# Kernel tuning notes

Measured on AMD Instinct MI355X. Metric: run time of the kernel, lower is better.

The kernel has to match this reference:

```python
import jax, jax.numpy as jnp
import numpy as np
import math

IMG_SIZE = 768
NUM_CLASSES = 90
THRESHOLD = 0.05
IOU_THRESHOLD = 0.5
MAX_DETECTIONS = 100
K_CAND = 512  # per-class candidate pool before greedy NMS
RATIOS = [(1.0, 1.0), (1.4, 0.7), (0.7, 1.4)]
SCALES = [2 ** 0, 2 ** (1.0 / 3.0), 2 ** (2.0 / 3.0)]


def _generate_anchors():
    anchor_scale = 4.0
    pyramid_levels = [3, 4, 5, 6, 7]
    all_levels = []
    for lv in pyramid_levels:
        stride = 2 ** lv
        size = anchor_scale * 2 ** lv
        grid = IMG_SIZE // stride
        sx = np.arange(grid) * stride
        sy, sx = np.meshgrid(np.arange(grid) * stride, sx, indexing='ij')
        # torch meshgrid(shift_y, shift_x, indexing='ij') -> rows are y
        yy, xx = np.meshgrid(np.arange(grid) * stride, np.arange(grid) * stride, indexing='ij')
        shifts = np.stack([xx.ravel(), yy.ravel(), xx.ravel(), yy.ravel()], axis=1).astype(np.float32)
        base = []
        for r in RATIOS:
            for s in SCALES:
                w = size * s * math.sqrt(r[0] / r[1])
                h = size * s * math.sqrt(r[1] / r[0])
                base.append([-w / 2, -h / 2, w / 2, h / 2])
        base = np.asarray(base, dtype=np.float32)  # [9,4]
        anc = (base[None, :, :] + shifts[:, None, :]).reshape(-1, 4)
        all_levels.append(anc)
    return np.concatenate(all_levels, axis=0)  # [110484,4]


def setup_inputs() -> dict:
    key = jax.random.key(0)
    k1, k2, k3 = jax.random.split(key, 3)
    A = 110484
    x = jax.random.normal(k1, (1, 3, IMG_SIZE, IMG_SIZE), dtype=jnp.float32)
    regression = jax.random.normal(k2, (1, A, 4), dtype=jnp.float32) * 0.3
    classification = jax.random.normal(k3, (1, A, NUM_CLASSES), dtype=jnp.float32) - 2.0
    anchors = jnp.asarray(_generate_anchors())
    return {"x": x, "regression": regression, "classification": classification, "anchors": anchors}


def _decode_and_clip(anchors, deltas, H, W):
    # BBoxTransform (RetinaNet-style): deltas = (dx, dy, dw, dh)
    wa = anchors[:, 2] - anchors[:, 0]
    ha = anchors[:, 3] - anchors[:, 1]
    cxa = anchors[:, 0] + 0.5 * wa
    cya = anchors[:, 1] + 0.5 * ha
    dx, dy, dw, dh = deltas[:, 0], deltas[:, 1], deltas[:, 2], deltas[:, 3]
    cx = cxa + dx * wa
    cy = cya + dy * ha
    w = jnp.exp(dw) * wa
    h = jnp.exp(dh) * ha
    x1 = jnp.clip(cx - 0.5 * w, 0.0, W)
    y1 = jnp.clip(cy - 0.5 * h, 0.0, H)
    x2 = jnp.clip(cx + 0.5 * w, 0.0, W)
    y2 = jnp.clip(cy + 0.5 * h, 0.0, H)
    return jnp.stack([x1, y1, x2, y2], axis=1)  # [A,4]


def _pairwise_iou(b):  # [K,4] -> [K,K]
    area = (b[:, 2] - b[:, 0]) * (b[:, 3] - b[:, 1])
    xx1 = jnp.maximum(b[:, None, 0], b[None, :, 0])
    yy1 = jnp.maximum(b[:, None, 1], b[None, :, 1])
    xx2 = jnp.minimum(b[:, None, 2], b[None, :, 2])
    yy2 = jnp.minimum(b[:, None, 3], b[None, :, 3])
    inter = jnp.clip(xx2 - xx1, 0.0) * jnp.clip(yy2 - yy1, 0.0)
    return inter / (area[:, None] + area[None, :] - inter + 1e-8)


def _greedy_nms(iou_c, valid_c):
    # boxes are pre-sorted by descending score; fixed-iteration greedy NMS
    def step(suppressed, i):
        keep_i = valid_c[i] & jnp.logical_not(suppressed[i])
        suppressed = jnp.where(keep_i, suppressed | (iou_c[i] > IOU_THRESHOLD), suppressed)
        return suppressed, keep_i
    _, keep = jax.lax.scan(step, jnp.zeros(iou_c.shape[0], dtype=bool), jnp.arange(iou_c.shape[0]))
    return keep  # [K]


def _postprocess(x, regression, classification, anchors):
    H, W = x.shape[2], x.shape[3]
    boxes = _decode_and_clip(anchors, regression[0], float(H), float(W))  # [A,4]
    scores = jax.nn.sigmoid(classification[0])                            # [A,C]
    # per-class top-K candidate pool (sorted desc), fixed-shape NMS
    vals, idx = jax.lax.top_k(scores.T, K_CAND)        # [C,K]
    cand = boxes[idx]                                   # [C,K,4]
    valid = vals > THRESHOLD                            # [C,K]
    iou = jax.vmap(_pairwise_iou)(cand)                 # [C,K,K]
    keep = jax.vmap(_greedy_nms)(iou, valid)            # [C,K]
    kept_scores = jnp.where(keep, vals, -1.0).reshape(-1)  # [C*K]
    top_vals, flat_idx = jax.lax.top_k(kept_scores, MAX_DETECTIONS)
    labels = (flat_idx // K_CAND).astype(jnp.float32)
    det_boxes = cand.reshape(-1, 4)[flat_idx]
    ok = top_vals > 0.0
    det = jnp.concatenate([
        jnp.zeros((MAX_DETECTIONS, 1), dtype=jnp.float32),  # batch ids (batch=1 -> 0)
        det_boxes,
        top_vals[:, None],
        labels[:, None],
    ], axis=1)  # [100,7]
    return jnp.where(ok[:, None], det, 0.0)


def reference(x, regression, classification, anchors):
    return _postprocess(x, regression, classification, anchors)
```

## Files before the change

kernel.cpp:

```cpp
#include <hip/hip_runtime.h>
#include <math.h>


#define A_N   110484
#define C_N   90
#define KCAND 512
#define NBINS 8192
#define KSH   19
#define MAXDET 100
#define IMG_F 768.0f
#define THRESH 0.05f
#define NS    4
#define VTOT  (A_N / 4)
#define VS4   ((VTOT + NS - 1) / NS)
#define SL_CAP 1024
#define CAND_N (NS * KCAND)
#define KEEP_CAP 100
#define T_BLKS ((A_N + 63) / 64)
#define S_BLKS (C_N * NS)
#define D_BLKS ((A_N + 255) / 256)
#define FCAP  512

typedef unsigned int u32;
typedef unsigned long long u64;

__device__ __forceinline__ u32 fkey(float f) {
    u32 u = __float_as_uint(f);
    return (u & 0x80000000u) ? ~u : (u | 0x80000000u);
}
__device__ __forceinline__ float unfkey(u32 k) {
    u32 u = (k & 0x80000000u) ? (k ^ 0x80000000u) : ~k;
    return __uint_as_float(u);
}
__device__ __forceinline__ u64 shflx64(u64 v, int m) {
    u32 lo = (u32)__shfl_xor((int)(u32)v, m, 64);
    u32 hi = (u32)__shfl_xor((int)(v >> 32), m, 64);
    return ((u64)hi << 32) | lo;
}

__global__ __launch_bounds__(256)
void prep_kernel(const float* __restrict__ cls,
                 u32* __restrict__ keysT) {
    __shared__ u32 tile[64 * 91];
    const int a0 = blockIdx.x * 64;
    const int lim = min(64, A_N - a0);
    const int n4 = (lim * C_N) >> 2;
    const float4* src4 = (const float4*)(cls + (size_t)a0 * C_N);
    for (int i4 = threadIdx.x; i4 < n4; i4 += 256) {
        float4 x4 = src4[i4];
        const u32 base = (u32)(4 * i4);
        float xs[4] = { x4.x, x4.y, x4.z, x4.w };
        #pragma unroll
        for (int k = 0; k < 4; ++k) {
            u32 i = base + k;
            u32 aa = i / C_N, c = i % C_N;
            float s = 1.0f / (1.0f + expf(-xs[k]));
            tile[aa * 91 + c] = fkey(s);
        }
    }
    __syncthreads();
    for (int j = threadIdx.x; j < C_N * 64; j += 256) {
        int c = j >> 6, aa = j & 63;
        if (aa < lim)
            keysT[(size_t)c * A_N + a0 + aa] = tile[aa * 91 + c];
    }
}

__global__ __launch_bounds__(256)
void select_kernel(const u32* __restrict__ keysT,
                   const float* __restrict__ anchors,
                   const float* __restrict__ reg,
                   float4* __restrict__ boxes,
                   u64* __restrict__ candbuf) {
    __shared__ u32 hist[NBINS];
    __shared__ u32 csum[256];
    __shared__ u64 lbuf[SL_CAP];
    __shared__ u32 sPv;
    __shared__ int lcnt;
    const int tid = threadIdx.x;

    if (blockIdx.x >= S_BLKS) {
        int a = (blockIdx.x - S_BLKS) * 256 + tid;
        if (a < A_N) {
            float4 an = ((const float4*)anchors)[a];
            float4 dl = ((const float4*)reg)[a];
            float wa = an.z - an.x, ha = an.w - an.y;
            float cx = an.x + 0.5f * wa + dl.x * wa;
            float cy = an.y + 0.5f * ha + dl.y * ha;
            float w = expf(dl.z) * wa;
            float h = expf(dl.w) * ha;
            float4 o;
            o.x = fminf(fmaxf(cx - 0.5f * w, 0.0f), IMG_F);
            o.y = fminf(fmaxf(cy - 0.5f * h, 0.0f), IMG_F);
            o.z = fminf(fmaxf(cx + 0.5f * w, 0.0f), IMG_F);
            o.w = fminf(fmaxf(cy + 0.5f * h, 0.0f), IMG_F);
            boxes[a] = o;
        }
        return;
    }
    const int c = blockIdx.x >> 2, s = blockIdx.x & 3;
    const int lo = s * VS4, hiEnd = min(VTOT, lo + VS4);
    const uint4* kv = (const uint4*)(keysT + (size_t)c * A_N);

    for (int i = tid; i < NBINS; i += 256) hist[i] = 0;
    if (tid == 0) { sPv = 0; lcnt = 0; }
    __syncthreads();
    for (int i = lo + tid; i < hiEnd; i += 256) {
        uint4 k = kv[i];
        atomicAdd(&hist[k.x >> KSH], 1u);
        atomicAdd(&hist[k.y >> KSH], 1u);
        atomicAdd(&hist[k.z >> KSH], 1u);
        atomicAdd(&hist[k.w >> KSH], 1u);
    }
    __syncthreads();
    u32 own = 0; const int hi = NBINS - 1 - 32 * tid;
    #pragma unroll 4
    for (int j = 0; j < 32; ++j) own += hist[hi - j];
    csum[tid] = own;
    __syncthreads();
    for (int off = 1; off < 256; off <<= 1) {
        u32 v = csum[tid];
        u32 a = (tid >= off) ? csum[tid - off] : 0u;
        __syncthreads();
        csum[tid] = v + a;
        __syncthreads();
    }
    const u32 incl = csum[tid], excl = incl - own;
    if (excl < (u32)KCAND && incl >= (u32)KCAND) {
        u32 cum = excl;
        for (int j = 0; j < 32; ++j) {
            u32 hv = hist[hi - j];
            if (cum + hv >= (u32)KCAND) { sPv = (u32)(hi - j); break; }
            cum += hv;
        }
    }
    __syncthreads();
    const u32 P = sPv;
    for (int i = lo + tid; i < hiEnd; i += 256) {
        uint4 k = kv[i];
        u32 base = (u32)(4 * i);
        if ((k.x >> KSH) >= P) {
            int p = atomicAdd(&lcnt, 1);
            if (p < SL_CAP) lbuf[p] = (((u64)(~k.x)) << 32) | base;
        }
        if ((k.y >> KSH) >= P) {
            int p = atomicAdd(&lcnt, 1);
            if (p < SL_CAP) lbuf[p] = (((u64)(~k.y)) << 32) | (base + 1);
        }
        if ((k.z >> KSH) >= P) {
            int p = atomicAdd(&lcnt, 1);
            if (p < SL_CAP) lbuf[p] = (((u64)(~k.z)) << 32) | (base + 2);
        }
        if ((k.w >> KSH) >= P) {
            int p = atomicAdd(&lcnt, 1);
            if (p < SL_CAP) lbuf[p] = (((u64)(~k.w)) << 32) | (base + 3);
        }
    }
    __syncthreads();
    const int n = min(lcnt, SL_CAP);
    for (int i = tid; i < SL_CAP; i += 256) if (i >= n) lbuf[i] = ~0ULL;
    __syncthreads();

    {
        const int l = tid & 63, w = tid >> 6;
        int ii[4]; u64 v[4];
        #pragma unroll
        for (int r = 0; r < 4; ++r) { ii[r] = 256 * w + 64 * r + l; v[r] = lbuf[ii[r]]; }
        __syncthreads();
        #pragma unroll
        for (u32 kk = 2; kk <= 1024; kk <<= 1) {
            #pragma unroll
            for (u32 j = kk >> 1; j > 0; j >>= 1) {
                if (j >= 256) {
                    #pragma unroll
                    for (int r = 0; r < 4; ++r) lbuf[ii[r]] = v[r];
                    __syncthreads();
                    #pragma unroll
                    for (int r = 0; r < 4; ++r) {
                        u64 pv = lbuf[ii[r] ^ j];
                        bool up = ((ii[r] & kk) == 0);
                        bool m = (((ii[r] & j) == 0) == up);
                        v[r] = m ? (v[r] < pv ? v[r] : pv) : (v[r] > pv ? v[r] : pv);
                    }
                    __syncthreads();
                } else if (j >= 64) {
                    const int rx = (int)(j >> 6);
                    u64 nv[4];
                    #pragma unroll
                    for (int r = 0; r < 4; ++r) {
                        u64 pv = v[r ^ rx];
                        bool up = ((ii[r] & kk) == 0);
                        bool m = (((ii[r] & j) == 0) == up);
                        nv[r] = m ? (v[r] < pv ? v[r] : pv) : (v[r] > pv ? v[r] : pv);
                    }
                    #pragma unroll
                    for (int r = 0; r < 4; ++r) v[r] = nv[r];
                } else {
                    #pragma unroll
                    for (int r = 0; r < 4; ++r) {
                        u64 pv = shflx64(v[r], (int)j);
                        bool up = ((ii[r] & kk) == 0);
                        bool m = (((ii[r] & j) == 0) == up);
                        v[r] = m ? (v[r] < pv ? v[r] : pv) : (v[r] > pv ? v[r] : pv);
                    }
                }
            }
        }
        u64* cb = candbuf + (size_t)c * CAND_N + (size_t)s * KCAND;
        const bool rev = (s & 1);
        #pragma unroll
        for (int r = 0; r < 4; ++r) {
            if (ii[r] < KCAND) {
                int d = rev ? (KCAND - 1 - ii[r]) : ii[r];
                cb[d] = v[r];
            }
        }
    }
}

__global__ __launch_bounds__(1024)
void snms_kernel(const u64* __restrict__ candbuf,
                 const float4* __restrict__ boxes,
                 u32* __restrict__ keptbuf, u32* __restrict__ cnt2) {
    __shared__ u64 sortbuf[2][CAND_N];
    __shared__ float bxx[KCAND], byy[KCAND], bzz[KCAND], bww[KCAND];
    __shared__ float ar[KCAND], sc[KCAND];
    __shared__ u32 keepf[16], wbase[17];
    u32* bmask = (u32*)&sortbuf[0][0];
    const int c = blockIdx.x, tid = threadIdx.x;
    const int l = tid & 63, w = tid >> 6;
    const int i0 = 128 * w + l, i1 = i0 + 64;

    const u64* cb = candbuf + (size_t)c * CAND_N;
    u64 v0 = cb[i0], v1 = cb[i1];
    int p = 0;
    #pragma unroll
    for (u32 kk = 1024; kk <= (u32)CAND_N; kk <<= 1) {
        #pragma unroll
        for (u32 j = kk >> 1; j > 0; j >>= 1) {
            if (j >= 128) {
                sortbuf[p][i0] = v0; sortbuf[p][i1] = v1;
                __syncthreads();
                u64 w0 = sortbuf[p][i0 ^ j], w1 = sortbuf[p][i1 ^ j];
                bool m0 = (((i0 & j) == 0) == ((i0 & kk) == 0));
                bool m1 = (((i1 & j) == 0) == ((i1 & kk) == 0));
                v0 = m0 ? (v0 < w0 ? v0 : w0) : (v0 > w0 ? v0 : w0);
                v1 = m1 ? (v1 < w1 ? v1 : w1) : (v1 > w1 ? v1 : w1);
                p ^= 1;
            } else if (j == 64) {
                bool up = ((i0 & kk) == 0);
                u64 mn = v0 < v1 ? v0 : v1, mx = v0 < v1 ? v1 : v0;
                v0 = up ? mn : mx; v1 = up ? mx : mn;
            } else {
                u64 w0 = shflx64(v0, (int)j), w1 = shflx64(v1, (int)j);
                bool m0 = (((i0 & j) == 0) == ((i0 & kk) == 0));
                bool m1 = (((i1 & j) == 0) == ((i1 & kk) == 0));
                v0 = m0 ? (v0 < w0 ? v0 : w0) : (v0 > w0 ? v0 : w0);
                v1 = m1 ? (v1 < w1 ? v1 : w1) : (v1 > w1 ? v1 : w1);
            }
        }
    }
    __syncthreads();

    if (w < 4) {
        u32 idx0 = (u32)v0, key0 = ~((u32)(v0 >> 32));
        u32 idx1 = (u32)v1, key1 = ~((u32)(v1 >> 32));
        sc[i0] = unfkey(key0); sc[i1] = unfkey(key1);
        float4 b0 = boxes[idx0], b1 = boxes[idx1];
        bxx[i0] = b0.x; byy[i0] = b0.y; bzz[i0] = b0.z; bww[i0] = b0.w;
        bxx[i1] = b1.x; byy[i1] = b1.y; bzz[i1] = b1.z; bww[i1] = b1.w;
        ar[i0] = (b0.z - b0.x) * (b0.w - b0.y);
        ar[i1] = (b1.z - b1.x) * (b1.w - b1.y);
    }
    for (int i = tid; i < KCAND * 16; i += 1024) bmask[i] = 0;
    if (tid < 16) keepf[tid] = 0;
    __syncthreads();

    {
        const int i = tid & (KCAND - 1);
        const int half = tid >> 9;
        const int count = (KCAND - 1) - i;
        const int j0 = i + 1 + (half ? (count >> 1) : 0);
        const int j1 = half ? KCAND : (i + 1 + (count >> 1));
        const float bix = bxx[i], biy = byy[i], biz = bzz[i], biw = bww[i];
        const float ai = ar[i];
        u32 m[16];
        #pragma unroll
        for (int q = 0; q < 16; ++q) m[q] = 0;
        for (int j = j0; j < j1; ++j) {
            float xx1 = fmaxf(bix, bxx[j]), yy1 = fmaxf(biy, byy[j]);
            float xx2 = fminf(biz, bzz[j]), yy2 = fminf(biw, bww[j]);
            float inter = fmaxf(xx2 - xx1, 0.0f) * fmaxf(yy2 - yy1, 0.0f);
            float uni = ai + ar[j] - inter + 1e-8f;
            if (inter > 0.5f * uni) m[j >> 5] |= (1u << (j & 31));
        }
        #pragma unroll
        for (int q = 0; q < 16; ++q)
            if (m[q]) atomicOr(&bmask[i * 16 + q], m[q]);
    }
    __syncthreads();

    if (tid < 64) {
        const int lw = tid & 15;
        u32 removed = 0, keepw = 0;
        u32 rA[8], rB[8]; float sA[8], sB[8];
        #pragma unroll
        for (int k = 0; k < 8; ++k) { rA[k] = bmask[k * 16 + lw]; sA[k] = sc[k]; }
        #pragma unroll 1
        for (int ch = 0; ch < 64; ch += 2) {
            const int tb1 = (ch + 1) * 8;
            #pragma unroll
            for (int k = 0; k < 8; ++k) { rB[k] = bmask[(tb1 + k) * 16 + lw]; sB[k] = sc[tb1 + k]; }
            {
                const int tb = ch * 8;
                #pragma unroll
                for (int k = 0; k < 8; ++k) {
                    const int t = tb + k;
                    u32 rw = (u32)__builtin_amdgcn_readlane((int)removed, t >> 5);
                    bool d = (sA[k] > THRESH) && (((rw >> (t & 31)) & 1u) == 0u);
                    removed |= d ? rA[k] : 0u;
                    keepw |= (d && (tid == (t >> 5))) ? (1u << (t & 31)) : 0u;
                }
            }
            const int tb2 = (ch + 2 < 64) ? (ch + 2) * 8 : 0;
            #pragma unroll
            for (int k = 0; k < 8; ++k) { rA[k] = bmask[(tb2 + k) * 16 + lw]; sA[k] = sc[tb2 + k]; }
            {
                #pragma unroll
                for (int k = 0; k < 8; ++k) {
                    const int t = tb1 + k;
                    u32 rw = (u32)__builtin_amdgcn_readlane((int)removed, t >> 5);
                    bool d = (sB[k] > THRESH) && (((rw >> (t & 31)) & 1u) == 0u);
                    removed |= d ? rB[k] : 0u;
                    keepw |= (d && (tid == (t >> 5))) ? (1u << (t & 31)) : 0u;
                }
            }
        }
        if (tid < 16) keepf[tid] = keepw;
    }
    __syncthreads();

    if (tid == 0) {
        u32 t = 0;
        for (int q = 0; q < 16; ++q) { wbase[q] = t; t += __popc(keepf[q]); }
        wbase[16] = t;
        cnt2[c] = (t < (u32)KEEP_CAP) ? t : (u32)KEEP_CAP;
    }
    __syncthreads();
    if (tid < KCAND) {
        u32 word = keepf[tid >> 5];
        u32 bit = (u32)tid & 31u;
        if ((word >> bit) & 1u) {
            u32 rank = wbase[tid >> 5] + __popc(word & ((1u << bit) - 1u));
            if (rank < (u32)KEEP_CAP) {
                float s = sc[tid];
                uint4 a, b;
                a.x = ~fkey(s);
                a.y = (u32)(c * KCAND + tid);
                a.z = __float_as_uint(bxx[tid]);
                a.w = __float_as_uint(byy[tid]);
                b.x = __float_as_uint(bzz[tid]);
                b.y = __float_as_uint(bww[tid]);
                b.z = __float_as_uint(s);
                b.w = 0u;
                uint4* e = (uint4*)(keptbuf + ((size_t)c * KEEP_CAP + rank) * 8);
                e[0] = a; e[1] = b;
            }
        }
    }
}

__global__ __launch_bounds__(1024)
void final_kernel(const u32* __restrict__ keptbuf, const u32* __restrict__ cnt2,
                  float* __restrict__ out) {
    __shared__ u32 hist[NBINS];
    __shared__ u32 csum[1024];
    __shared__ u64 ebuf[FCAP];
    __shared__ u32 eidx[FCAP];
    __shared__ u32 scnt[C_N];
    __shared__ u32 sP;
    __shared__ int sN;
    const int tid = threadIdx.x;
    const int TOT = C_N * KEEP_CAP;

    for (int i = tid; i < MAXDET * 7; i += 1024) out[i] = 0.0f;
    for (int i = tid; i < NBINS; i += 1024) hist[i] = 0;
    if (tid < C_N) scnt[tid] = cnt2[tid];
    if (tid == 0) { sN = 0; sP = NBINS - 1; }
    __syncthreads();

    for (int i = tid; i < TOT; i += 1024) {
        u32 c = (u32)i / KEEP_CAP, pp = (u32)i % KEEP_CAP;
        if (pp < scnt[c]) {
            u32 khi = keptbuf[(size_t)i * 8];
            atomicAdd(&hist[khi >> KSH], 1u);
        }
    }
    __syncthreads();
    u32 own = 0; const int lo = 8 * tid;
    #pragma unroll
    for (int j = 0; j < 8; ++j) own += hist[lo + j];
    csum[tid] = own;
    __syncthreads();
    for (int off = 1; off < 1024; off <<= 1) {
        u32 v = csum[tid];
        u32 a = (tid >= off) ? csum[tid - off] : 0u;
        __syncthreads();
        csum[tid] = v + a;
        __syncthreads();
    }
    const u32 incl = csum[tid], excl = incl - own;
    if (excl < (u32)MAXDET && incl >= (u32)MAXDET) {
        u32 cum = excl;
        for (int j = 0; j < 8; ++j) {
            u32 h = hist[lo + j];
            if (cum + h >= (u32)MAXDET) { sP = (u32)(lo + j); break; }
            cum += h;
        }
    }
    __syncthreads();
    const u32 P = sP;
    for (int i = tid; i < TOT; i += 1024) {
        u32 c = (u32)i / KEEP_CAP, pp = (u32)i % KEEP_CAP;
        if (pp < scnt[c]) {
            const uint2 v2 = *((const uint2*)(keptbuf + (size_t)i * 8));
            if ((v2.x >> KSH) <= P) {
                int p = atomicAdd(&sN, 1);
                if (p < FCAP) {
                    ebuf[p] = ((u64)v2.x << 32) | v2.y;
                    eidx[p] = (u32)i;
                }
            }
        }
    }
    __syncthreads();
    const int n = min(sN, FCAP);
    u32 m = 128; while ((int)m < n) m <<= 1;
    for (int i = tid; i < (int)m; i += 1024) if (i >= n) ebuf[i] = ~0ULL;
    __syncthreads();
    for (u32 kk = 2; kk <= m; kk <<= 1) {
        for (u32 j = kk >> 1; j > 0; j >>= 1) {
            u32 i = (u32)tid;
            if (i < m) {
                u32 ixj = i ^ j;
                if (ixj > i) {
                    u64 x = ebuf[i], y = ebuf[ixj];
                    bool up = ((i & kk) == 0);
                    if (up ? (x > y) : (x < y)) {
                        ebuf[i] = y; ebuf[ixj] = x;
                        u32 t = eidx[i]; eidx[i] = eidx[ixj]; eidx[ixj] = t;
                    }
                }
            }
            __syncthreads();
        }
    }
    if (tid < MAXDET && tid < n) {
        u64 comp = ebuf[tid];
        if (comp != ~0ULL) {
            const uint4* e = (const uint4*)(keptbuf + (size_t)eidx[tid] * 8);
            uint4 a = e[0], b = e[1];
            float* o = out + tid * 7;
            o[0] = 0.0f;
            o[1] = __uint_as_float(a.z); o[2] = __uint_as_float(a.w);
            o[3] = __uint_as_float(b.x); o[4] = __uint_as_float(b.y);
            o[5] = __uint_as_float(b.z);
            o[6] = (float)(((u32)comp) >> 9);
        }
    }
}

extern "C" void kernel_launch(void* const* d_in, const int* in_sizes, int n_in,
                              void* d_out, int out_size, void* d_ws, size_t ws_size,
                              hipStream_t stream) {
    const float* reg     = (const float*)d_in[1];
    const float* cls     = (const float*)d_in[2];
    const float* anchors = (const float*)d_in[3];
    float* out = (float*)d_out;

    char* ws = (char*)d_ws;
    size_t off = 0;
    auto alloc = [&](size_t bytes) -> void* {
        void* p = ws + off;
        off = (off + bytes + 255) & ~(size_t)255;
        return p;
    };
    u32*    keysT   = (u32*)   alloc((size_t)C_N * A_N * sizeof(u32));
    float4* boxes   = (float4*)alloc((size_t)A_N * sizeof(float4));
    u64*    candbuf = (u64*)   alloc((size_t)C_N * CAND_N * sizeof(u64));
    u32*    keptbuf = (u32*)   alloc((size_t)C_N * KEEP_CAP * 8 * sizeof(u32));
    u32*    cnt2    = (u32*)   alloc((size_t)C_N * sizeof(u32));
    (void)ws_size;

    prep_kernel<<<T_BLKS, 256, 0, stream>>>(cls, keysT);
    select_kernel<<<S_BLKS + D_BLKS, 256, 0, stream>>>(keysT, anchors, reg, boxes, candbuf);
    snms_kernel<<<C_N, 1024, 0, stream>>>(candbuf, boxes, keptbuf, cnt2);
    final_kernel<<<1, 1024, 0, stream>>>(keptbuf, cnt2, out);
}
```

Measured before the change: 217.6 us.

## Split per-class NMS into sort, parallel IoU-mask, and scan kernels

The monolithic per-class snms kernel becomes three kernels. A sort kernel writes the sorted boxes and scores to global memory. A mask kernel uses four blocks per class, with each wave building IoU suppression rows through ballots instead of per-thread loops and shared-memory atomics. A scan kernel reloads the mask and runs the greedy scan. This spreads the O(K^2) IoU work across more blocks and removes the uneven triangular per-thread loop, at the cost of two extra launches and global round-trips for the mask and boxes.

```diff
diff --git a/kernel.cpp b/kernel.cpp
--- a/kernel.cpp
+++ b/kernel.cpp
@@ -20,6 +20,7 @@
 #define S_BLKS (C_N * NS)
 #define D_BLKS ((A_N + 255) / 256)
 #define FCAP  512
+#define STRIPS 4
 
 typedef unsigned int u32;
 typedef unsigned long long u64;
@@ -219,14 +220,10 @@
 }
 
 __global__ __launch_bounds__(1024)
-void snms_kernel(const u64* __restrict__ candbuf,
+void sort_kernel(const u64* __restrict__ candbuf,
                  const float4* __restrict__ boxes,
-                 u32* __restrict__ keptbuf, u32* __restrict__ cnt2) {
+                 float4* __restrict__ sbox, float* __restrict__ ssc) {
     __shared__ u64 sortbuf[2][CAND_N];
-    __shared__ float bxx[KCAND], byy[KCAND], bzz[KCAND], bww[KCAND];
-    __shared__ float ar[KCAND], sc[KCAND];
-    __shared__ u32 keepf[16], wbase[17];
-    u32* bmask = (u32*)&sortbuf[0][0];
     const int c = blockIdx.x, tid = threadIdx.x;
     const int l = tid & 63, w = tid >> 6;
     const int i0 = 128 * w + l, i1 = i0 + 64;
@@ -260,44 +257,67 @@
             }
         }
     }
-    __syncthreads();
-
     if (w < 4) {
         u32 idx0 = (u32)v0, key0 = ~((u32)(v0 >> 32));
         u32 idx1 = (u32)v1, key1 = ~((u32)(v1 >> 32));
-        sc[i0] = unfkey(key0); sc[i1] = unfkey(key1);
-        float4 b0 = boxes[idx0], b1 = boxes[idx1];
-        bxx[i0] = b0.x; byy[i0] = b0.y; bzz[i0] = b0.z; bww[i0] = b0.w;
-        bxx[i1] = b1.x; byy[i1] = b1.y; bzz[i1] = b1.z; bww[i1] = b1.w;
-        ar[i0] = (b0.z - b0.x) * (b0.w - b0.y);
-        ar[i1] = (b1.z - b1.x) * (b1.w - b1.y);
-    }
-    for (int i = tid; i < KCAND * 16; i += 1024) bmask[i] = 0;
+        ssc[(size_t)c * KCAND + i0] = unfkey(key0);
+        ssc[(size_t)c * KCAND + i1] = unfkey(key1);
+        sbox[(size_t)c * KCAND + i0] = boxes[idx0];
+        sbox[(size_t)c * KCAND + i1] = boxes[idx1];
+    }
+}
+
+__global__ __launch_bounds__(256)
+void mask_kernel(const float4* __restrict__ sbox, u32* __restrict__ gmask) {
+    __shared__ float4 bb[KCAND];
+    const int c = blockIdx.x >> 2, s = blockIdx.x & 3;
+    const int tid = threadIdx.x;
+    const int l = tid & 63, wv = tid >> 6;
+    const float4* sb = sbox + (size_t)c * KCAND;
+    for (int i = tid; i < KCAND; i += 256) bb[i] = sb[i];
+    __syncthreads();
+    const int wid = 4 * s + wv;
+    u32* gm = gmask + (size_t)c * KCAND * 16;
+    for (int r = wid; r < KCAND; r += 16) {
+        const float4 bi = bb[r];
+        const float ai = (bi.z - bi.x) * (bi.w - bi.y);
+        const int q0 = (r + 1) >> 6;
+        u32* row = gm + r * 16;
+        if (l < 2 * q0) row[l] = 0;
+        for (int q = q0; q < 8; ++q) {
+            const int j = q * 64 + l;
+            const float4 bj = bb[j];
+            float xx1 = fmaxf(bi.x, bj.x), yy1 = fmaxf(bi.y, bj.y);
+            float xx2 = fminf(bi.z, bj.z), yy2 = fminf(bi.w, bj.w);
+            float inter = fmaxf(xx2 - xx1, 0.0f) * fmaxf(yy2 - yy1, 0.0f);
+            float aj = (bj.z - bj.x) * (bj.w - bj.y);
+            float uni = ai + aj - inter + 1e-8f;
+            bool sup = (j > r) && (inter > 0.5f * uni);
+            u64 bal = __ballot(sup);
+            if (l == 0)      row[2 * q]     = (u32)bal;
+            else if (l == 1) row[2 * q + 1] = (u32)(bal >> 32);
+        }
+    }
+}
+
+__global__ __launch_bounds__(512)
+void scan_kernel(const u32* __restrict__ gmask,
+                 const float4* __restrict__ sbox,
+                 const float* __restrict__ ssc,
+                 u32* __restrict__ keptbuf, u32* __restrict__ cnt2) {
+    __shared__ u32 bmask[KCAND * 16];
+    __shared__ float sc[KCAND];
+    __shared__ float4 bb[KCAND];
+    __shared__ u32 keepf[16], wbase[17];
+    const int c = blockIdx.x, tid = threadIdx.x;
+
+    const uint4* gm4 = (const uint4*)(gmask + (size_t)c * KCAND * 16);
+    uint4* bm4 = (uint4*)bmask;
+    #pragma unroll
+    for (int i = 0; i < 4; ++i) bm4[tid + 512 * i] = gm4[tid + 512 * i];
+    sc[tid] = ssc[(size_t)c * KCAND + tid];
+    bb[tid] = sbox[(size_t)c * KCAND + tid];
     if (tid < 16) keepf[tid] = 0;
-    __syncthreads();
-
-    {
-        const int i = tid & (KCAND - 1);
-        const int half = tid >> 9;
-        const int count = (KCAND - 1) - i;
-        const int j0 = i + 1 + (half ? (count >> 1) : 0);
-        const int j1 = half ? KCAND : (i + 1 + (count >> 1));
-        const float bix = bxx[i], biy = byy[i], biz = bzz[i], biw = bww[i];
-        const float ai = ar[i];
-        u32 m[16];
-        #pragma unroll
-        for (int q = 0; q < 16; ++q) m[q] = 0;
-        for (int j = j0; j < j1; ++j) {
-            float xx1 = fmaxf(bix, bxx[j]), yy1 = fmaxf(biy, byy[j]);
-            float xx2 = fminf(biz, bzz[j]), yy2 = fminf(biw, bww[j]);
-            float inter = fmaxf(xx2 - xx1, 0.0f) * fmaxf(yy2 - yy1, 0.0f);
-            float uni = ai + ar[j] - inter + 1e-8f;
-            if (inter > 0.5f * uni) m[j >> 5] |= (1u << (j & 31));
-        }
-        #pragma unroll
-        for (int q = 0; q < 16; ++q)
-            if (m[q]) atomicOr(&bmask[i * 16 + q], m[q]);
-    }
     __syncthreads();
 
     if (tid < 64) {
@@ -347,24 +367,25 @@
         cnt2[c] = (t < (u32)KEEP_CAP) ? t : (u32)KEEP_CAP;
     }
     __syncthreads();
-    if (tid < KCAND) {
+    {
         u32 word = keepf[tid >> 5];
         u32 bit = (u32)tid & 31u;
         if ((word >> bit) & 1u) {
             u32 rank = wbase[tid >> 5] + __popc(word & ((1u << bit) - 1u));
             if (rank < (u32)KEEP_CAP) {
                 float s = sc[tid];
-                uint4 a, b;
-                a.x = ~fkey(s);
-                a.y = (u32)(c * KCAND + tid);
-                a.z = __float_as_uint(bxx[tid]);
-                a.w = __float_as_uint(byy[tid]);
-                b.x = __float_as_uint(bzz[tid]);
-                b.y = __float_as_uint(bww[tid]);
-                b.z = __float_as_uint(s);
-                b.w = 0u;
+                float4 b = bb[tid];
+                uint4 a2, b2;
+                a2.x = ~fkey(s);
+                a2.y = (u32)(c * KCAND + tid);
+                a2.z = __float_as_uint(b.x);
+                a2.w = __float_as_uint(b.y);
+                b2.x = __float_as_uint(b.z);
+                b2.y = __float_as_uint(b.w);
+                b2.z = __float_as_uint(s);
+                b2.w = 0u;
                 uint4* e = (uint4*)(keptbuf + ((size_t)c * KEEP_CAP + rank) * 8);
-                e[0] = a; e[1] = b;
+                e[0] = a2; e[1] = b2;
             }
         }
     }
@@ -490,10 +511,15 @@
     u64*    candbuf = (u64*)   alloc((size_t)C_N * CAND_N * sizeof(u64));
     u32*    keptbuf = (u32*)   alloc((size_t)C_N * KEEP_CAP * 8 * sizeof(u32));
     u32*    cnt2    = (u32*)   alloc((size_t)C_N * sizeof(u32));
+    float4* sbox    = (float4*)alloc((size_t)C_N * KCAND * sizeof(float4));
+    float*  ssc     = (float*) alloc((size_t)C_N * KCAND * sizeof(float));
+    u32*    gmask   = (u32*)   alloc((size_t)C_N * KCAND * 16 * sizeof(u32));
     (void)ws_size;
 
     prep_kernel<<<T_BLKS, 256, 0, stream>>>(cls, keysT);
     select_kernel<<<S_BLKS + D_BLKS, 256, 0, stream>>>(keysT, anchors, reg, boxes, candbuf);
-    snms_kernel<<<C_N, 1024, 0, stream>>>(candbuf, boxes, keptbuf, cnt2);
+    sort_kernel<<<C_N, 1024, 0, stream>>>(candbuf, boxes, sbox, ssc);
+    mask_kernel<<<C_N * STRIPS, 256, 0, stream>>>(sbox, gmask);
+    scan_kernel<<<C_N, 512, 0, stream>>>(gmask, sbox, ssc, keptbuf, cnt2);
     final_kernel<<<1, 1024, 0, stream>>>(keptbuf, cnt2, out);
 }
```

New measurement: 226.0 us. 3.9% more time.
